# Kernel optimization log

Measured on AMD Instinct MI355X. Metric: run time of the kernel, lower is better.

Reference implementation:

```python
import jax, jax.numpy as jnp
import numpy as np

B, C, T = 8, 64, 2048


def setup_inputs() -> dict:
    key = jax.random.key(0)
    eeg_data = jax.random.normal(key, (B, C, T), dtype=jnp.float32)
    return {"eeg_data": eeg_data}


def _hilbert(signal):
    # FFT-based analytic signal, faithful to the torch code:
    # zero frequencies >= n//2 (even n) or >= (n+1)//2 (odd n), then multiply ALL by 2.
    n = signal.shape[-1]
    spec = jnp.fft.fft(signal, axis=-1)
    cut = n // 2 if n % 2 == 0 else (n + 1) // 2
    keep = (jnp.arange(n) < cut).astype(spec.dtype)
    spec = spec * keep * 2
    return jnp.fft.ifft(spec, axis=-1)


def reference(eeg_data):
    b, c, t = eeg_data.shape
    analytic = _hilbert(eeg_data)
    phase = jnp.angle(analytic)                      # [B, C, T]
    # pairwise phase differences: [B, C, C, T]
    phase_diff = phase[:, :, None, :] - phase[:, None, :, :]
    sin_pd = jnp.sin(phase_diff)
    numerator = jnp.abs(jnp.mean(sin_pd, axis=-1))   # [B, C, C]
    denominator = jnp.mean(jnp.abs(sin_pd), axis=-1)
    denominator = jnp.where(denominator == 0, jnp.float32(1e-8), denominator)
    wpli = numerator / denominator
    eye_mask = 1.0 - jnp.eye(c, dtype=wpli.dtype)[None, :, :]
    return wpli * eye_mask
```

## Files before the change

### kernel.cpp

```cpp
#include <hip/hip_runtime.h>
#include <math.h>

#define T_LEN 2048
#define C_CH  64
#define B_N   8

__global__ __launch_bounds__(256) void hilbert_phasor_kernel(
    const float* __restrict__ x, float2* __restrict__ phasor) {
  __shared__ float2 bufA[T_LEN];
  __shared__ float2 bufB[T_LEN];

  const int bc = blockIdx.x;
  const float* sig = x + (size_t)bc * T_LEN;

  for (int t = threadIdx.x; t < T_LEN; t += 256)
    bufA[t] = make_float2(sig[t], 0.0f);
  __syncthreads();

  float2* src = bufA;
  float2* dst = bufB;

  for (int n = T_LEN, s = 1, ls = 0; n >= 2; n >>= 1, s <<= 1, ++ls) {
    const int m = n >> 1;
    const float theta0 = -6.28318530717958647692f / (float)n;
    for (int idx = threadIdx.x; idx < T_LEN / 2; idx += 256) {
      const int p = idx >> ls;
      const int q = idx & (s - 1);
      const float ang = theta0 * (float)p;
      float sn, cs;
      __sincosf(ang, &sn, &cs);
      const float2 a = src[q + s * p];
      const float2 b = src[q + s * (p + m)];
      const float2 sum = make_float2(a.x + b.x, a.y + b.y);
      const float2 dif = make_float2(a.x - b.x, a.y - b.y);
      dst[q + s * (2 * p)]     = sum;
      dst[q + s * (2 * p + 1)] = make_float2(dif.x * cs - dif.y * sn,
                                             dif.x * sn + dif.y * cs);
    }
    __syncthreads();
    float2* tmp = src; src = dst; dst = tmp;
  }

  for (int k = threadIdx.x; k < T_LEN; k += 256) {
    const float f = (k < T_LEN / 2) ? 2.0f : 0.0f;
    src[k].x *= f;
    src[k].y *= f;
  }
  __syncthreads();

  for (int n = T_LEN, s = 1, ls = 0; n >= 2; n >>= 1, s <<= 1, ++ls) {
    const int m = n >> 1;
    const float theta0 = 6.28318530717958647692f / (float)n;
    for (int idx = threadIdx.x; idx < T_LEN / 2; idx += 256) {
      const int p = idx >> ls;
      const int q = idx & (s - 1);
      const float ang = theta0 * (float)p;
      float sn, cs;
      __sincosf(ang, &sn, &cs);
      const float2 a = src[q + s * p];
      const float2 b = src[q + s * (p + m)];
      const float2 sum = make_float2(a.x + b.x, a.y + b.y);
      const float2 dif = make_float2(a.x - b.x, a.y - b.y);
      dst[q + s * (2 * p)]     = sum;
      dst[q + s * (2 * p + 1)] = make_float2(dif.x * cs - dif.y * sn,
                                             dif.x * sn + dif.y * cs);
    }
    __syncthreads();
    float2* tmp = src; src = dst; dst = tmp;
  }

  for (int t = threadIdx.x; t < T_LEN; t += 256) {
    const float2 z = src[t];
    const float mag2 = z.x * z.x + z.y * z.y;
    float u, v;
    if (mag2 > 0.0f) {
      const float inv = rsqrtf(mag2);
      u = z.x * inv;
      v = z.y * inv;
    } else {
      u = 1.0f;
      v = 0.0f;
    }
    phasor[(size_t)bc * T_LEN + t] = make_float2(u, v);
  }
}

__global__ __launch_bounds__(256) void wpli_pair_kernel(
    const float2* __restrict__ phasor, float* __restrict__ out) {
  const int blk = blockIdx.x;
  const int b  = blk >> 12;
  const int ij = blk & 4095;
  const int i  = ij >> 6;
  const int j  = ij & 63;
  if (i >= j) return;

  const float2* pi = phasor + ((size_t)(b * C_CH + i)) * T_LEN;
  const float2* pj = phasor + ((size_t)(b * C_CH + j)) * T_LEN;

  float num = 0.0f, den = 0.0f;
  for (int t = threadIdx.x; t < T_LEN; t += 256) {
    const float2 zi = pi[t];
    const float2 zj = pj[t];
    const float s = zi.y * zj.x - zi.x * zj.y;
    num += s;
    den += fabsf(s);
  }

  for (int off = 32; off > 0; off >>= 1) {
    num += __shfl_down(num, off, 64);
    den += __shfl_down(den, off, 64);
  }
  __shared__ float red[8];
  const int lane = threadIdx.x & 63;
  const int wave = threadIdx.x >> 6;
  if (lane == 0) { red[wave * 2] = num; red[wave * 2 + 1] = den; }
  __syncthreads();
  if (threadIdx.x == 0) {
    float n2 = 0.0f, d2 = 0.0f;
    for (int w = 0; w < 4; ++w) { n2 += red[w * 2]; d2 += red[w * 2 + 1]; }
    const float wv = (d2 > 0.0f) ? fabsf(n2) / d2 : 0.0f;
    out[((size_t)b * C_CH + i) * C_CH + j] = wv;
    out[((size_t)b * C_CH + j) * C_CH + i] = wv;
  }
}

extern "C" void kernel_launch(void* const* d_in, const int* in_sizes, int n_in,
                              void* d_out, int out_size, void* d_ws, size_t ws_size,
                              hipStream_t stream) {
  const float* eeg = (const float*)d_in[0];
  float* out = (float*)d_out;
  float2* phasor = (float2*)d_ws;

  hipMemsetAsync(d_out, 0, (size_t)out_size * sizeof(float), stream);

  hilbert_phasor_kernel<<<B_N * C_CH, 256, 0, stream>>>(eeg, phasor);
  wpli_pair_kernel<<<B_N * C_CH * C_CH, 256, 0, stream>>>(phasor, out);
}
```

Measured before the change: 121.0 us.

## Tile pairwise wPLI with shared-memory register blocking and use radix-4 FFT

Replaces the one-block-per-channel-pair wPLI kernel, which reloaded both phasor rows for every pair, with a tiled kernel. Each block stages 32 time samples for all 64 channels in shared memory and computes a 4x4 register tile of pair sums, with the time axis split into chunks whose partials a finalize kernel reduces. The Hilbert FFT moves from radix-2 to radix-4 stages, roughly halving the barrier-separated passes. In exchange it computes both triangles of the symmetric pair matrix and adds partial-sum workspace traffic plus an extra launch.

```diff
diff --git a/kernel.cpp b/kernel.cpp
--- a/kernel.cpp
+++ b/kernel.cpp
@@ -4,6 +4,64 @@
 #define T_LEN 2048
 #define C_CH  64
 #define B_N   8
+
+__device__ __forceinline__ float2 cadd(float2 a, float2 b) { return make_float2(a.x + b.x, a.y + b.y); }
+__device__ __forceinline__ float2 csub(float2 a, float2 b) { return make_float2(a.x - b.x, a.y - b.y); }
+
+template <int SIGN>
+__device__ __forceinline__ void fft_stages(float2*& src, float2*& dst, int tid) {
+  for (int n = T_LEN, ls = 0; n >= 4; n >>= 2, ls += 2) {
+    const int s = 1 << ls;
+    const int m = n >> 2;
+    const float th = (float)SIGN * 6.28318530717958647692f / (float)n;
+    for (int idx = tid; idx < T_LEN / 4; idx += 256) {
+      const int p = idx >> ls;
+      const int q = idx & (s - 1);
+      const int base = q + s * p;
+      const float2 a = src[base];
+      const float2 b = src[base + s * m];
+      const float2 c = src[base + 2 * s * m];
+      const float2 d = src[base + 3 * s * m];
+      const float2 t0 = cadd(a, c);
+      const float2 t1 = csub(a, c);
+      const float2 t2 = cadd(b, d);
+      const float2 t3 = csub(b, d);
+      const float2 y0 = cadd(t0, t2);
+      const float2 r2 = csub(t0, t2);
+      float2 r1, r3;
+      if (SIGN < 0) {
+        r1 = make_float2(t1.x + t3.y, t1.y - t3.x);
+        r3 = make_float2(t1.x - t3.y, t1.y + t3.x);
+      } else {
+        r1 = make_float2(t1.x - t3.y, t1.y + t3.x);
+        r3 = make_float2(t1.x + t3.y, t1.y - t3.x);
+      }
+      const float pf = (float)p;
+      float s1, c1, s2, c2, s3, c3;
+      __sincosf(th * pf, &s1, &c1);
+      __sincosf(2.0f * th * pf, &s2, &c2);
+      __sincosf(3.0f * th * pf, &s3, &c3);
+      const float2 y1 = make_float2(r1.x * c1 - r1.y * s1, r1.x * s1 + r1.y * c1);
+      const float2 y2 = make_float2(r2.x * c2 - r2.y * s2, r2.x * s2 + r2.y * c2);
+      const float2 y3 = make_float2(r3.x * c3 - r3.y * s3, r3.x * s3 + r3.y * c3);
+      const int ob = q + s * 4 * p;
+      dst[ob]         = y0;
+      dst[ob + s]     = y1;
+      dst[ob + 2 * s] = y2;
+      dst[ob + 3 * s] = y3;
+    }
+    __syncthreads();
+    float2* tmp = src; src = dst; dst = tmp;
+  }
+  for (int q = tid; q < T_LEN / 2; q += 256) {
+    const float2 a = src[q];
+    const float2 b = src[q + T_LEN / 2];
+    dst[q]             = cadd(a, b);
+    dst[q + T_LEN / 2] = csub(a, b);
+  }
+  __syncthreads();
+  float2* tmp = src; src = dst; dst = tmp;
+}
 
 __global__ __launch_bounds__(256) void hilbert_phasor_kernel(
     const float* __restrict__ x, float2* __restrict__ phasor) {
@@ -11,65 +69,28 @@
   __shared__ float2 bufB[T_LEN];
 
   const int bc = blockIdx.x;
+  const int tid = threadIdx.x;
   const float* sig = x + (size_t)bc * T_LEN;
 
-  for (int t = threadIdx.x; t < T_LEN; t += 256)
+  for (int t = tid; t < T_LEN; t += 256)
     bufA[t] = make_float2(sig[t], 0.0f);
   __syncthreads();
 
   float2* src = bufA;
   float2* dst = bufB;
 
-  for (int n = T_LEN, s = 1, ls = 0; n >= 2; n >>= 1, s <<= 1, ++ls) {
-    const int m = n >> 1;
-    const float theta0 = -6.28318530717958647692f / (float)n;
-    for (int idx = threadIdx.x; idx < T_LEN / 2; idx += 256) {
-      const int p = idx >> ls;
-      const int q = idx & (s - 1);
-      const float ang = theta0 * (float)p;
-      float sn, cs;
-      __sincosf(ang, &sn, &cs);
-      const float2 a = src[q + s * p];
-      const float2 b = src[q + s * (p + m)];
-      const float2 sum = make_float2(a.x + b.x, a.y + b.y);
-      const float2 dif = make_float2(a.x - b.x, a.y - b.y);
-      dst[q + s * (2 * p)]     = sum;
-      dst[q + s * (2 * p + 1)] = make_float2(dif.x * cs - dif.y * sn,
-                                             dif.x * sn + dif.y * cs);
-    }
-    __syncthreads();
-    float2* tmp = src; src = dst; dst = tmp;
-  }
-
-  for (int k = threadIdx.x; k < T_LEN; k += 256) {
+  fft_stages<-1>(src, dst, tid);
+
+  for (int k = tid; k < T_LEN; k += 256) {
     const float f = (k < T_LEN / 2) ? 2.0f : 0.0f;
     src[k].x *= f;
     src[k].y *= f;
   }
   __syncthreads();
 
-  for (int n = T_LEN, s = 1, ls = 0; n >= 2; n >>= 1, s <<= 1, ++ls) {
-    const int m = n >> 1;
-    const float theta0 = 6.28318530717958647692f / (float)n;
-    for (int idx = threadIdx.x; idx < T_LEN / 2; idx += 256) {
-      const int p = idx >> ls;
-      const int q = idx & (s - 1);
-      const float ang = theta0 * (float)p;
-      float sn, cs;
-      __sincosf(ang, &sn, &cs);
-      const float2 a = src[q + s * p];
-      const float2 b = src[q + s * (p + m)];
-      const float2 sum = make_float2(a.x + b.x, a.y + b.y);
-      const float2 dif = make_float2(a.x - b.x, a.y - b.y);
-      dst[q + s * (2 * p)]     = sum;
-      dst[q + s * (2 * p + 1)] = make_float2(dif.x * cs - dif.y * sn,
-                                             dif.x * sn + dif.y * cs);
-    }
-    __syncthreads();
-    float2* tmp = src; src = dst; dst = tmp;
-  }
-
-  for (int t = threadIdx.x; t < T_LEN; t += 256) {
+  fft_stages<1>(src, dst, tid);
+
+  for (int t = tid; t < T_LEN; t += 256) {
     const float2 z = src[t];
     const float mag2 = z.x * z.x + z.y * z.y;
     float u, v;
@@ -85,43 +106,79 @@
   }
 }
 
-__global__ __launch_bounds__(256) void wpli_pair_kernel(
-    const float2* __restrict__ phasor, float* __restrict__ out) {
-  const int blk = blockIdx.x;
-  const int b  = blk >> 12;
-  const int ij = blk & 4095;
-  const int i  = ij >> 6;
-  const int j  = ij & 63;
-  if (i >= j) return;
-
-  const float2* pi = phasor + ((size_t)(b * C_CH + i)) * T_LEN;
-  const float2* pj = phasor + ((size_t)(b * C_CH + j)) * T_LEN;
-
-  float num = 0.0f, den = 0.0f;
-  for (int t = threadIdx.x; t < T_LEN; t += 256) {
-    const float2 zi = pi[t];
-    const float2 zj = pj[t];
-    const float s = zi.y * zj.x - zi.x * zj.y;
-    num += s;
-    den += fabsf(s);
-  }
-
-  for (int off = 32; off > 0; off >>= 1) {
-    num += __shfl_down(num, off, 64);
-    den += __shfl_down(den, off, 64);
-  }
-  __shared__ float red[8];
-  const int lane = threadIdx.x & 63;
-  const int wave = threadIdx.x >> 6;
-  if (lane == 0) { red[wave * 2] = num; red[wave * 2 + 1] = den; }
-  __syncthreads();
-  if (threadIdx.x == 0) {
-    float n2 = 0.0f, d2 = 0.0f;
-    for (int w = 0; w < 4; ++w) { n2 += red[w * 2]; d2 += red[w * 2 + 1]; }
-    const float wv = (d2 > 0.0f) ? fabsf(n2) / d2 : 0.0f;
-    out[((size_t)b * C_CH + i) * C_CH + j] = wv;
-    out[((size_t)b * C_CH + j) * C_CH + i] = wv;
-  }
+__global__ __launch_bounds__(256) void wpli_partial_kernel(
+    const float2* __restrict__ phasor, float2* __restrict__ part, int nchunk) {
+  __shared__ float lu[32][65];
+  __shared__ float lv[32][65];
+
+  const int c = blockIdx.x;
+  const int b = blockIdx.y;
+  const int tid = threadIdx.x;
+  const int tx = tid & 15;
+  const int ty = tid >> 4;
+
+  float accn[4][4] = {{0}}, accd[4][4] = {{0}};
+
+  for (int sub = c; sub < T_LEN / 32; sub += nchunk) {
+    const int t0 = sub * 32;
+    __syncthreads();
+    for (int idx = tid; idx < 2048; idx += 256) {
+      const int ch = idx >> 5;
+      const int tt = idx & 31;
+      const float2 z = phasor[((size_t)(b * C_CH + ch)) * T_LEN + t0 + tt];
+      lu[tt][ch] = z.x;
+      lv[tt][ch] = z.y;
+    }
+    __syncthreads();
+
+    for (int tt = 0; tt < 32; ++tt) {
+      float ui[4], vi[4], uj[4], vj[4];
+#pragma unroll
+      for (int a = 0; a < 4; ++a) {
+        ui[a] = lu[tt][ty * 4 + a];
+        vi[a] = lv[tt][ty * 4 + a];
+        uj[a] = lu[tt][tx * 4 + a];
+        vj[a] = lv[tt][tx * 4 + a];
+      }
+#pragma unroll
+      for (int a = 0; a < 4; ++a)
+#pragma unroll
+        for (int e = 0; e < 4; ++e) {
+          const float s = vi[a] * uj[e] - ui[a] * vj[e];
+          accn[a][e] += s;
+          accd[a][e] += fabsf(s);
+        }
+    }
+  }
+
+  float2* dstp = part + ((size_t)c * B_N + b) * (C_CH * C_CH);
+#pragma unroll
+  for (int a = 0; a < 4; ++a)
+#pragma unroll
+    for (int e = 0; e < 4; ++e) {
+      const int i = ty * 4 + a;
+      const int j = tx * 4 + e;
+      dstp[i * C_CH + j] = make_float2(accn[a][e], accd[a][e]);
+    }
+}
+
+__global__ __launch_bounds__(256) void wpli_finalize_kernel(
+    const float2* __restrict__ part, float* __restrict__ out, int nchunk) {
+  const int idx = blockIdx.x * 256 + threadIdx.x;
+  if (idx >= B_N * C_CH * C_CH) return;
+  const int b = idx >> 12;
+  const int pair = idx & 4095;
+  float n = 0.0f, d = 0.0f;
+  for (int c = 0; c < nchunk; ++c) {
+    const float2 p = part[((size_t)c * B_N + b) * (C_CH * C_CH) + pair];
+    n += p.x;
+    d += p.y;
+  }
+  const int i = pair >> 6;
+  const int j = pair & 63;
+  float w = (d > 0.0f) ? fabsf(n) / d : 0.0f;
+  if (i == j) w = 0.0f;
+  out[idx] = w;
 }
 
 extern "C" void kernel_launch(void* const* d_in, const int* in_sizes, int n_in,
@@ -129,10 +186,21 @@
                               hipStream_t stream) {
   const float* eeg = (const float*)d_in[0];
   float* out = (float*)d_out;
+
+  const size_t phasor_bytes = (size_t)B_N * C_CH * T_LEN * sizeof(float2);
   float2* phasor = (float2*)d_ws;
-
-  hipMemsetAsync(d_out, 0, (size_t)out_size * sizeof(float), stream);
+  float2* part = (float2*)((char*)d_ws + phasor_bytes);
+
+  const size_t per_chunk = (size_t)B_N * C_CH * C_CH * sizeof(float2);
+  const size_t avail = (ws_size > phasor_bytes) ? ws_size - phasor_bytes : 0;
+  int nchunk = 64;
+  while (nchunk > 1 && (size_t)nchunk * per_chunk > avail) nchunk >>= 1;
 
   hilbert_phasor_kernel<<<B_N * C_CH, 256, 0, stream>>>(eeg, phasor);
-  wpli_pair_kernel<<<B_N * C_CH * C_CH, 256, 0, stream>>>(phasor, out);
-}
+
+  dim3 grid(nchunk, B_N);
+  wpli_partial_kernel<<<grid, 256, 0, stream>>>(phasor, part, nchunk);
+
+  wpli_finalize_kernel<<<(B_N * C_CH * C_CH + 255) / 256, 256, 0, stream>>>(
+      part, out, nchunk);
+}
```

New measurement: 104.2 us. 13.9% less time.
